# Performance work log

Hardware: AMD Instinct MI355X
Metric: run time of the kernel (lower is better)

Reference implementation:

```python
import jax, jax.numpy as jnp
import numpy as np

B, K, H, W = 8, 1024, 24, 24
C = H * W            # in_channels = 576
NH = 6               # hardcoded num_heads
HD = C // NH         # 96


def setup_inputs() -> dict:
    key = jax.random.key(0)
    ks = jax.random.split(key, 8)
    s = 1.0 / np.sqrt(C)
    return {
        "input1": jax.random.normal(ks[0], (B, K, H, W), jnp.float32),
        "input2": jax.random.normal(ks[1], (B, K, H, W), jnp.float32),
        "Wq": jax.random.uniform(ks[2], (C, C), jnp.float32, -s, s),
        "bq": jax.random.uniform(ks[3], (C,), jnp.float32, -s, s),
        "Wk": jax.random.uniform(ks[4], (C, C), jnp.float32, -s, s),
        "bk": jax.random.uniform(ks[5], (C,), jnp.float32, -s, s),
        "Wv": jax.random.uniform(ks[6], (C, C), jnp.float32, -s, s),
        "bv": jax.random.uniform(ks[7], (C,), jnp.float32, -s, s),
    }


def reference(input1, input2, Wq, bq, Wk, bk, Wv, bv):
    b, k, h, w = input1.shape
    c = h * w
    x1 = input1.reshape(b, k, c)
    x2 = input2.reshape(b, k, c)
    # torch nn.Linear: y = x @ W^T + b
    q = x1 @ Wq.T + bq                      # [b, k, c]
    kk = x2 @ Wk.T + bk
    v = x2 @ Wv.T + bv
    # torch .view scrambles: [b, k, c] -> [b, NH, c//NH, k] (row-major reshape)
    q = q.reshape(b, NH, c // NH, k)
    kk = kk.reshape(b, NH, c // NH, k)
    v = v.reshape(b, NH, c // NH, k)
    # scores = q^T k over head-dim; NOTE: no 1/sqrt(d) scaling in original
    scores = jnp.einsum('bhdq,bhdk->bhqk', q, kk)   # [b, NH, k, k]
    weights = jax.nn.softmax(scores, axis=-1)
    # context = value @ weights^T -> [b, NH, hd, k]
    ctx = jnp.einsum('bhdk,bhqk->bhdq', v, weights)
    return ctx.reshape(b, k, h, w)
```

## Files before the change

kernel.cpp:

```cpp
#include <hip/hip_runtime.h>
#include <cmath>

#define BATCH 8
#define KDIM  1024
#define CH    576
#define NHEAD 6
#define HDIM  96

typedef _Float16 f16;
typedef f16 f16x4 __attribute__((ext_vector_type(4)));
typedef f16 f16x8 __attribute__((ext_vector_type(8)));
typedef float f32x16 __attribute__((ext_vector_type(16)));
typedef unsigned int u32;

#define PSZ  (BATCH * KDIM * CH)
#define WSZ  (CH * CH)

__device__ inline f32x16 zero16() {
    f32x16 z;
#pragma unroll
    for (int r = 0; r < 16; ++r) z[r] = 0.f;
    return z;
}

__global__ __launch_bounds__(256) void convert_w(
    const float* __restrict__ Wq, const float* __restrict__ Wk,
    const float* __restrict__ Wv, f16* __restrict__ wh)
{
    int idx = blockIdx.x * 256 + threadIdx.x;
    if (idx >= 3 * WSZ / 8) return;
    int seg = idx / (WSZ / 8);
    const float* src = (seg == 0) ? Wq : (seg == 1) ? Wk : Wv;
    f16* dst = wh + seg * WSZ;
    idx -= seg * (WSZ / 8);
    float4 u0 = ((const float4*)src)[2 * idx];
    float4 u1 = ((const float4*)src)[2 * idx + 1];
    f16x8 hv;
    hv[0] = (f16)u0.x; hv[1] = (f16)u0.y; hv[2] = (f16)u0.z; hv[3] = (f16)u0.w;
    hv[4] = (f16)u1.x; hv[5] = (f16)u1.y; hv[6] = (f16)u1.z; hv[7] = (f16)u1.w;
    ((f16x8*)dst)[idx] = hv;
}

__global__ __launch_bounds__(256, 4) void proj_kernel(
    const float* __restrict__ x1, const float* __restrict__ x2,
    const f16* __restrict__ wh,
    const float* __restrict__ bq, const float* __restrict__ bk,
    const float* __restrict__ bv,
    f16* __restrict__ qf, f16* __restrict__ kf, f16* __restrict__ vf)
{
    const int bid = blockIdx.x;
    const int k8  = bid & 7;
    const int j   = bid >> 3;
    const int xb  = j % 3;
    const int z   = (j / 3) % 3;
    const int y   = k8 + 8 * (j / 9);

    const float* A    = (z == 0) ? x1 : x2;
    const f16* W      = wh + z * WSZ;
    const float* bias = (z == 0) ? bq : (z == 1) ? bk : bv;
    f16* dst          = (z == 0) ? qf : (z == 1) ? kf : vf;

    __shared__ f16 As[64 * 72];
    __shared__ f16 Ws[192 * 72];

    const int tid = threadIdx.x;
    const int lane = tid & 63, w = tid >> 6;
    const int l31 = lane & 31, half = lane >> 5;
    const int mw = 32 * (w & 1), nh = 96 * (w >> 1);
    const int nBase = xb * 192;
    const int mBase = y * 64;

    int arow[2], ach[2], wrow[6], wch[6];
#pragma unroll
    for (int r = 0; r < 2; ++r) {
        int idx = r * 256 + tid;
        arow[r] = idx >> 3; ach[r] = idx & 7;
    }
#pragma unroll
    for (int r = 0; r < 6; ++r) {
        int idx = r * 256 + tid;
        wrow[r] = idx >> 3; wch[r] = idx & 7;
    }

    float4 aP[2][2];
    f16x8 wP[6];
#pragma unroll
    for (int r = 0; r < 2; ++r) {
        const float* p = &A[(size_t)(mBase + arow[r]) * CH + ach[r] * 8];
        aP[r][0] = ((const float4*)p)[0];
        aP[r][1] = ((const float4*)p)[1];
    }
#pragma unroll
    for (int r = 0; r < 6; ++r)
        wP[r] = *(const f16x8*)&W[(size_t)(nBase + wrow[r]) * CH + wch[r] * 8];

    f32x16 acc[3] = {zero16(), zero16(), zero16()};

    for (int k0 = 0; k0 < CH; k0 += 64) {
        __syncthreads();
#pragma unroll
        for (int r = 0; r < 2; ++r) {
            f16x8 hv;
            hv[0] = (f16)aP[r][0].x; hv[1] = (f16)aP[r][0].y;
            hv[2] = (f16)aP[r][0].z; hv[3] = (f16)aP[r][0].w;
            hv[4] = (f16)aP[r][1].x; hv[5] = (f16)aP[r][1].y;
            hv[6] = (f16)aP[r][1].z; hv[7] = (f16)aP[r][1].w;
            *(f16x8*)&As[arow[r] * 72 + ach[r] * 8] = hv;
        }
#pragma unroll
        for (int r = 0; r < 6; ++r)
            *(f16x8*)&Ws[wrow[r] * 72 + wch[r] * 8] = wP[r];
        __syncthreads();
        if (k0 + 64 < CH) {
#pragma unroll
            for (int r = 0; r < 2; ++r) {
                const float* p = &A[(size_t)(mBase + arow[r]) * CH + k0 + 64 + ach[r] * 8];
                aP[r][0] = ((const float4*)p)[0];
                aP[r][1] = ((const float4*)p)[1];
            }
#pragma unroll
            for (int r = 0; r < 6; ++r)
                wP[r] = *(const f16x8*)&W[(size_t)(nBase + wrow[r]) * CH + k0 + 64 + wch[r] * 8];
        }
#pragma unroll
        for (int ks = 0; ks < 4; ++ks) {
            f16x8 a = *(const f16x8*)&As[(mw + l31) * 72 + 16 * ks + 8 * half];
#pragma unroll
            for (int nt = 0; nt < 3; ++nt) {
                f16x8 bfr = *(const f16x8*)&Ws[(nh + 32 * nt + l31) * 72 + 16 * ks + 8 * half];
                acc[nt] = __builtin_amdgcn_mfma_f32_32x32x16_f16(a, bfr, acc[nt], 0, 0, 0);
            }
        }
    }

#pragma unroll
    for (int nt = 0; nt < 3; ++nt) {
        int n = nBase + nh + 32 * nt + l31;
        float bsv = bias[n];
#pragma unroll
        for (int r = 0; r < 16; ++r) {
            int m = mBase + mw + (r & 3) + 8 * (r >> 2) + 4 * half;
            dst[(size_t)m * CH + n] = (f16)(acc[nt][r] + bsv);
        }
    }
}

__global__ __launch_bounds__(256) void repack_qkv(
    const f16* __restrict__ qf, const f16* __restrict__ kf,
    const f16* __restrict__ vf,
    f16* __restrict__ QF, f16* __restrict__ KF, f16* __restrict__ VF)
{
    const int tt = blockIdx.x;
    const int bh = blockIdx.y;
    const int z  = blockIdx.z;
    const int tid = threadIdx.x;

    if (z < 2) {
        const f16* src = z ? kf : qf;
        f16* dst = z ? KF : QF;

        __shared__ f16 Ts[96 * 72];
        const int rowbase = (bh / NHEAD) * CH + (bh % NHEAD) * HDIM;

#pragma unroll
        for (int r = 0; r < 3; ++r) {
            int idx = r * 256 + tid;
            int d = idx >> 3, g = idx & 7;
            *(f16x8*)&Ts[d * 72 + g * 8] =
                *(const f16x8*)&src[(size_t)(rowbase + d) * KDIM + tt * 64 + g * 8];
        }
        __syncthreads();

        f16* dblk = dst + ((size_t)bh * 16 + tt) * 6144;
#pragma unroll
        for (int r = 0; r < 3; ++r) {
            int c = r * 256 + tid;
            int lane = c & 63;
            int ks = (c >> 6) % 6;
            int jg = c / 384;
            int l31 = lane & 31, half = lane >> 5;
            int jl = jg * 32 + l31;
            int d0 = ks * 16 + half * 8;
            f16x8 v;
#pragma unroll
            for (int u = 0; u < 8; ++u) v[u] = Ts[(d0 + u) * 72 + jl];
            *(f16x8*)&dblk[(size_t)c * 8] = v;
        }
    } else {
        const f16* vbase = vf + ((size_t)(bh / NHEAD) * CH + (bh % NHEAD) * HDIM) * KDIM;
        f16* dblk = VF + ((size_t)bh * 16 + tt) * 6144;

#pragma unroll
        for (int r = 0; r < 3; ++r) {
            int c = r * 256 + tid;
            int lane = c & 63;
            int t  = (c >> 6) % 3;
            int kq = ((c >> 6) / 3) & 1;
            int jg = c / 384;
            int l31 = lane & 31, half = lane >> 5;
            int d = t * 32 + l31;
            int j = tt * 64 + jg * 32 + kq * 16 + half * 8;
            f16x8 v = *(const f16x8*)&vbase[(size_t)d * KDIM + j];
            *(f16x8*)&dblk[(size_t)c * 8] = v;
        }
    }
}

__global__ __launch_bounds__(256, 3) void attn_kernel(
    const f16* __restrict__ QF, const f16* __restrict__ KF,
    const f16* __restrict__ VF, float* __restrict__ out)
{
    __shared__ __align__(16) char smem[25600];

    const int bh = blockIdx.x;
    const int qt = blockIdx.y;
    const int h  = bh % NHEAD;
    const int b  = bh / NHEAD;

    const int tid = threadIdx.x;
    const int lane = tid & 63, w = tid >> 6;
    const int ih = w & 1, jg = w >> 1;
    const int l31 = lane & 31, half = lane >> 5;
    const int iw = 32 * ih;

    const f16* Qblk  = QF + ((size_t)bh * 16 + qt) * 6144 + (size_t)ih * 3072 + (size_t)lane * 8;
    const f16* Kfrag = KF + (size_t)bh * 16 * 6144 + (size_t)jg * 3072 + (size_t)lane * 8;
    const f16* Vfrag = VF + (size_t)bh * 16 * 6144 + (size_t)jg * 3072 + (size_t)lane * 8;

    f16x8 qfr[6];
#pragma unroll
    for (int ks = 0; ks < 6; ++ks) {
        qfr[ks] = *(const f16x8*)&Qblk[ks * 512];
#pragma unroll
        for (int u = 0; u < 8; ++u)
            qfr[ks][u] = (f16)((float)qfr[ks][u] * 1.44269504f);
    }

    f16x8 kc[6], vc[6];
#pragma unroll
    for (int ks = 0; ks < 6; ++ks)
        kc[ks] = *(const f16x8*)&Kfrag[ks * 512];
#pragma unroll
    for (int kq = 0; kq < 2; ++kq)
#pragma unroll
        for (int t = 0; t < 3; ++t)
            vc[kq * 3 + t] = *(const f16x8*)&Vfrag[kq * 1536 + t * 512];

    float l_run = 0.f;
    f32x16 Oacc[3] = {zero16(), zero16(), zero16()};

    for (int jt = 0; jt < 16; ++jt) {
        f32x16 s0 = zero16();
#pragma unroll
        for (int ks = 0; ks < 6; ++ks)
            s0 = __builtin_amdgcn_mfma_f32_32x32x16_f16(kc[ks], qfr[ks], s0, 0, 0, 0);

        if (jt + 1 < 16) {
            const f16* Kt = Kfrag + (size_t)(jt + 1) * 6144;
#pragma unroll
            for (int ks = 0; ks < 6; ++ks)
                kc[ks] = *(const f16x8*)&Kt[ks * 512];
        }

        f16x4 pq[4];
#pragma unroll
        for (int r = 0; r < 16; ++r) {
            float e = __builtin_amdgcn_exp2f(s0[r] - 26.0f);
            l_run += e;
            pq[r >> 2][r & 3] = (f16)e;
        }

#pragma unroll
        for (int kq = 0; kq < 2; ++kq) {
            union { f16x4 h; u32 u[2]; } snd, rcv, keep;
            keep.h = half ? pq[2 * kq + 1] : pq[2 * kq];
            snd.h  = half ? pq[2 * kq]     : pq[2 * kq + 1];
            rcv.u[0] = __shfl_xor((int)snd.u[0], 32);
            rcv.u[1] = __shfl_xor((int)snd.u[1], 32);
            f16x8 bp;
            if (half == 0) {
#pragma unroll
                for (int v = 0; v < 4; ++v) { bp[v] = keep.h[v]; bp[4 + v] = rcv.h[v]; }
            } else {
#pragma unroll
                for (int v = 0; v < 4; ++v) { bp[v] = rcv.h[v]; bp[4 + v] = keep.h[v]; }
            }
#pragma unroll
            for (int t = 0; t < 3; ++t)
                Oacc[t] = __builtin_amdgcn_mfma_f32_32x32x16_f16(vc[kq * 3 + t], bp, Oacc[t], 0, 0, 0);
        }

        if (jt + 1 < 16) {
            const f16* Vt = Vfrag + (size_t)(jt + 1) * 6144;
#pragma unroll
            for (int kq = 0; kq < 2; ++kq)
#pragma unroll
                for (int t = 0; t < 3; ++t)
                    vc[kq * 3 + t] = *(const f16x8*)&Vt[kq * 1536 + t * 512];
        }
    }

    l_run += __shfl_xor(l_run, 32);

    float* Oscr = (float*)smem;
    float* lScr = (float*)(smem + 25344);
    if (jg == 1) {
        if (half == 0) lScr[iw + l31] = l_run;
        float* od = Oscr + ih * 3168;
#pragma unroll
        for (int t = 0; t < 3; ++t)
#pragma unroll
            for (int r = 0; r < 16; ++r) {
                int d = 32 * t + (r & 3) + 8 * (r >> 2) + 4 * half;
                od[d * 33 + l31] = Oacc[t][r];
            }
    }
    __syncthreads();
    if (jg == 0) {
        float linv = 1.0f / (l_run + lScr[iw + l31]);
        const float* od = Oscr + ih * 3168;
        float* obase = out + ((size_t)b * CH + (size_t)h * HDIM) * KDIM
                           + qt * 64 + iw + l31;
#pragma unroll
        for (int t = 0; t < 3; ++t)
#pragma unroll
            for (int r = 0; r < 16; ++r) {
                int d = 32 * t + (r & 3) + 8 * (r >> 2) + 4 * half;
                obase[(size_t)d * KDIM] =
                    (Oacc[t][r] + od[d * 33 + l31]) * linv;
            }
    }
}

extern "C" void kernel_launch(void* const* d_in, const int* in_sizes, int n_in,
                              void* d_out, int out_size, void* d_ws, size_t ws_size,
                              hipStream_t stream)
{
    const float* x1 = (const float*)d_in[0];
    const float* x2 = (const float*)d_in[1];
    const float* Wq = (const float*)d_in[2];
    const float* bq = (const float*)d_in[3];
    const float* Wk = (const float*)d_in[4];
    const float* bk = (const float*)d_in[5];
    const float* Wv = (const float*)d_in[6];
    const float* bv = (const float*)d_in[7];
    float* out = (float*)d_out;

    const size_t P = PSZ;
    f16* qf = (f16*)d_ws;
    f16* kf = qf + P;
    f16* vf = kf + P;
    f16* QF = vf + P;
    f16* KF = QF + P;
    f16* VF = KF + P;
    f16* wh = VF + P;

    convert_w<<<486, 256, 0, stream>>>(Wq, Wk, Wv, wh);

    proj_kernel<<<1152, 256, 0, stream>>>(x1, x2, wh, bq, bk, bv, qf, kf, vf);

    dim3 rgrid(KDIM / 64, BATCH * NHEAD, 3);
    repack_qkv<<<rgrid, 256, 0, stream>>>(qf, kf, vf, QF, KF, VF);

    dim3 agrid(BATCH * NHEAD, KDIM / 64);
    attn_kernel<<<agrid, 256, 0, stream>>>(QF, KF, VF, out);
}
```

Before: 159.6 us.

## Prepack weights into MFMA fragment order and load B operands directly from global

The weight conversion kernel now writes fp16 weights pre-swizzled into the per-lane MFMA B-fragment layout, tiled by output block and k-chunk. The projection GEMM then drops its shared-memory weight tile and loads each wave's B fragments straight from global into registers, with a one-chunk register prefetch. This removes LDS stores and loads, and shared memory pressure, for the weight operand. In exchange it adds register pressure (12 f16x8 fragments per thread), duplicates weight loads across waves that share columns, and makes the conversion kernel more complex.

```diff
diff --git a/kernel.cpp b/kernel.cpp
--- a/kernel.cpp
+++ b/kernel.cpp
@@ -23,22 +23,41 @@
     return z;
 }
 
-__global__ __launch_bounds__(256) void convert_w(
+__global__ __launch_bounds__(256) void convert_w2(
     const float* __restrict__ Wq, const float* __restrict__ Wk,
     const float* __restrict__ Wv, f16* __restrict__ wh)
 {
-    int idx = blockIdx.x * 256 + threadIdx.x;
-    if (idx >= 3 * WSZ / 8) return;
-    int seg = idx / (WSZ / 8);
-    const float* src = (seg == 0) ? Wq : (seg == 1) ? Wk : Wv;
-    f16* dst = wh + seg * WSZ;
-    idx -= seg * (WSZ / 8);
-    float4 u0 = ((const float4*)src)[2 * idx];
-    float4 u1 = ((const float4*)src)[2 * idx + 1];
-    f16x8 hv;
-    hv[0] = (f16)u0.x; hv[1] = (f16)u0.y; hv[2] = (f16)u0.z; hv[3] = (f16)u0.w;
-    hv[4] = (f16)u1.x; hv[5] = (f16)u1.y; hv[6] = (f16)u1.z; hv[7] = (f16)u1.w;
-    ((f16x8*)dst)[idx] = hv;
+    const int k0 = blockIdx.x;
+    const int xb = blockIdx.y;
+    const int z  = blockIdx.z;
+    const float* src = (z == 0) ? Wq : (z == 1) ? Wk : Wv;
+    const int tid = threadIdx.x;
+
+    __shared__ f16 Ws2[192 * 88];
+
+#pragma unroll
+    for (int r = 0; r < 12; ++r) {
+        int idx = r * 256 + tid;
+        int row = idx >> 4, c4 = idx & 15;
+        float4 u = *(const float4*)&src[(size_t)(xb * 192 + row) * CH + k0 * 64 + c4 * 4];
+        f16x4 hv;
+        hv[0] = (f16)u.x; hv[1] = (f16)u.y; hv[2] = (f16)u.z; hv[3] = (f16)u.w;
+        *(f16x4*)&Ws2[row * 88 + c4 * 4] = hv;
+    }
+    __syncthreads();
+
+    f16* dst = wh + ((size_t)((z * 3 + xb) * 9 + k0) * 24) * 512;
+#pragma unroll
+    for (int rr = 0; rr < 6; ++rr) {
+        int cc = rr * 256 + tid;
+        int lc = cc >> 6, lane = cc & 63;
+        int ks = lc / 6, rem = lc % 6;
+        int hw = rem / 3, nt = rem % 3;
+        int n_local = hw * 96 + nt * 32 + (lane & 31);
+        int kk = ks * 16 + (lane >> 5) * 8;
+        f16x8 v = *(const f16x8*)&Ws2[n_local * 88 + kk];
+        *(f16x8*)&dst[(size_t)cc * 8] = v;
+    }
 }
 
 __global__ __launch_bounds__(256, 4) void proj_kernel(
@@ -56,12 +75,10 @@
     const int y   = k8 + 8 * (j / 9);
 
     const float* A    = (z == 0) ? x1 : x2;
-    const f16* W      = wh + z * WSZ;
     const float* bias = (z == 0) ? bq : (z == 1) ? bk : bv;
     f16* dst          = (z == 0) ? qf : (z == 1) ? kf : vf;
 
     __shared__ f16 As[64 * 72];
-    __shared__ f16 Ws[192 * 72];
 
     const int tid = threadIdx.x;
     const int lane = tid & 63, w = tid >> 6;
@@ -70,33 +87,34 @@
     const int nBase = xb * 192;
     const int mBase = y * 64;
 
-    int arow[2], ach[2], wrow[6], wch[6];
+    int arow[2], ach[2];
 #pragma unroll
     for (int r = 0; r < 2; ++r) {
         int idx = r * 256 + tid;
         arow[r] = idx >> 3; ach[r] = idx & 7;
     }
-#pragma unroll
-    for (int r = 0; r < 6; ++r) {
-        int idx = r * 256 + tid;
-        wrow[r] = idx >> 3; wch[r] = idx & 7;
-    }
+
+    const f16* Wfrag = wh + ((size_t)(z * 3 + xb) * 216 + (size_t)(w >> 1) * 3) * 512
+                          + (size_t)lane * 8;
 
     float4 aP[2][2];
-    f16x8 wP[6];
 #pragma unroll
     for (int r = 0; r < 2; ++r) {
         const float* p = &A[(size_t)(mBase + arow[r]) * CH + ach[r] * 8];
         aP[r][0] = ((const float4*)p)[0];
         aP[r][1] = ((const float4*)p)[1];
     }
-#pragma unroll
-    for (int r = 0; r < 6; ++r)
-        wP[r] = *(const f16x8*)&W[(size_t)(nBase + wrow[r]) * CH + wch[r] * 8];
+
+    f16x8 wc[12];
+#pragma unroll
+    for (int ks = 0; ks < 4; ++ks)
+#pragma unroll
+        for (int nt = 0; nt < 3; ++nt)
+            wc[ks * 3 + nt] = *(const f16x8*)&Wfrag[(size_t)(ks * 6 + nt) * 512];
 
     f32x16 acc[3] = {zero16(), zero16(), zero16()};
 
-    for (int k0 = 0; k0 < CH; k0 += 64) {
+    for (int k0i = 0; k0i < 9; ++k0i) {
         __syncthreads();
 #pragma unroll
         for (int r = 0; r < 2; ++r) {
@@ -107,29 +125,29 @@
             hv[6] = (f16)aP[r][1].z; hv[7] = (f16)aP[r][1].w;
             *(f16x8*)&As[arow[r] * 72 + ach[r] * 8] = hv;
         }
-#pragma unroll
-        for (int r = 0; r < 6; ++r)
-            *(f16x8*)&Ws[wrow[r] * 72 + wch[r] * 8] = wP[r];
         __syncthreads();
-        if (k0 + 64 < CH) {
+        if (k0i + 1 < 9) {
 #pragma unroll
             for (int r = 0; r < 2; ++r) {
-                const float* p = &A[(size_t)(mBase + arow[r]) * CH + k0 + 64 + ach[r] * 8];
+                const float* p = &A[(size_t)(mBase + arow[r]) * CH + (k0i + 1) * 64 + ach[r] * 8];
                 aP[r][0] = ((const float4*)p)[0];
                 aP[r][1] = ((const float4*)p)[1];
             }
-#pragma unroll
-            for (int r = 0; r < 6; ++r)
-                wP[r] = *(const f16x8*)&W[(size_t)(nBase + wrow[r]) * CH + k0 + 64 + wch[r] * 8];
         }
 #pragma unroll
         for (int ks = 0; ks < 4; ++ks) {
             f16x8 a = *(const f16x8*)&As[(mw + l31) * 72 + 16 * ks + 8 * half];
 #pragma unroll
-            for (int nt = 0; nt < 3; ++nt) {
-                f16x8 bfr = *(const f16x8*)&Ws[(nh + 32 * nt + l31) * 72 + 16 * ks + 8 * half];
-                acc[nt] = __builtin_amdgcn_mfma_f32_32x32x16_f16(a, bfr, acc[nt], 0, 0, 0);
-            }
+            for (int nt = 0; nt < 3; ++nt)
+                acc[nt] = __builtin_amdgcn_mfma_f32_32x32x16_f16(a, wc[ks * 3 + nt], acc[nt], 0, 0, 0);
+        }
+        if (k0i + 1 < 9) {
+            const f16* Wn = Wfrag + (size_t)(k0i + 1) * 24 * 512;
+#pragma unroll
+            for (int ks = 0; ks < 4; ++ks)
+#pragma unroll
+                for (int nt = 0; nt < 3; ++nt)
+                    wc[ks * 3 + nt] = *(const f16x8*)&Wn[(size_t)(ks * 6 + nt) * 512];
         }
     }
 
@@ -355,7 +373,8 @@
     f16* VF = KF + P;
     f16* wh = VF + P;
 
-    convert_w<<<486, 256, 0, stream>>>(Wq, Wk, Wv, wh);
+    dim3 wgrid(9, 3, 3);
+    convert_w2<<<wgrid, 256, 0, stream>>>(Wq, Wk, Wv, wh);
 
     proj_kernel<<<1152, 256, 0, stream>>>(x1, x2, wh, bq, bk, bv, qf, kf, vf);
 
```

Result: slower. 205.9 us (+29.0%).
